# Kernel optimization log

Measured on AMD Instinct MI355X. Metric: run time of the kernel, lower is better.

## Reference

```python
import jax, jax.numpy as jnp
import numpy as np

B, S, DIM, H = 2, 2048, 1024, 16
DH = DIM // H


def setup_inputs() -> dict:
    key = jax.random.key(0)
    ks = jax.random.split(key, 12)
    sd = 0.02
    inp = {
        "query": jax.random.normal(ks[0], (B, S, DIM), jnp.float32),
        "key": jax.random.normal(ks[1], (B, S, DIM), jnp.float32),
        "value": jax.random.normal(ks[2], (B, S, DIM), jnp.float32),
        "pad_mask": jax.random.randint(ks[3], (B, 1, 1, S), 0, 2, jnp.int32),
        "training_status": 1,
        "Wq": jax.random.normal(ks[4], (DIM, DIM), jnp.float32) * sd,
        "bq": jnp.zeros((DIM,), jnp.float32),
        "Wk": jax.random.normal(ks[5], (DIM, DIM), jnp.float32) * sd,
        "bk": jnp.zeros((DIM,), jnp.float32),
        "Wv": jax.random.normal(ks[6], (DIM, DIM), jnp.float32) * sd,
        "bv": jnp.zeros((DIM,), jnp.float32),
        "Wf": jax.random.normal(ks[7], (DIM, DIM), jnp.float32) * sd,
        "bf": jnp.zeros((DIM,), jnp.float32),
    }
    return inp


def reference(query, key, value, pad_mask, training_status, Wq, bq, Wk, bk, Wv, bv, Wf, bf):
    b, s, _ = query.shape
    # projections, split heads -> [B, H, S, Dh]
    def split_heads(x):
        return x.reshape(b, -1, H, DH).transpose(0, 2, 1, 3)

    q = split_heads(query @ Wq + bq)
    k = split_heads(key @ Wk + bk)
    v = split_heads(value @ Wv + bv)

    # NOTE: original divides by sqrt(Dh) twice (explicit + self.scale) => /Dh
    scores = jnp.einsum("bhqd,bhkd->bhqk", q, k) / jnp.asarray(DH, q.dtype)
    if training_status:
        scores = jnp.where(pad_mask == 0, jnp.asarray(-1e9, scores.dtype), scores)
    attn = jax.nn.softmax(scores, axis=-1)
    out = jnp.einsum("bhqk,bhkd->bhqd", attn, v)  # [B,H,S,Dh]
    out = out.transpose(0, 2, 1, 3).reshape(b, s, DIM)
    return out @ Wf + bf
```

## Files before the change

kernel.cpp:

```cpp
#include <hip/hip_runtime.h>

#define Bn   2
#define Sn   2048
#define DIMn 1024
#define Hn   16
#define DHn  64

typedef unsigned short u16;
typedef unsigned int   u32;

typedef __attribute__((ext_vector_type(8))) __bf16 bf16x8;
typedef __attribute__((ext_vector_type(8))) float  f32x8v;
typedef __attribute__((ext_vector_type(4))) float  f32x4;

__device__ __forceinline__ u16 f2bf(float f) {
    union { float f; u32 u; } v; v.f = f;
    u32 r = v.u + 0x7fffu + ((v.u >> 16) & 1u);
    return (u16)(r >> 16);
}
__device__ __forceinline__ bf16x8 ldfrag(const u16* p) {
    union { uint4 u; bf16x8 v; } x;
    x.u = *(const uint4*)p;
    return x.v;
}
__device__ __forceinline__ uint4 pack8(const u16 h[8]) {
    uint4 r;
    r.x = (u32)h[0] | ((u32)h[1] << 16);
    r.y = (u32)h[2] | ((u32)h[3] << 16);
    r.z = (u32)h[4] | ((u32)h[5] << 16);
    r.w = (u32)h[6] | ((u32)h[7] << 16);
    return r;
}
__device__ __forceinline__ void gl_lds16(const void* g, void* l) {
    __builtin_amdgcn_global_load_lds(
        (const __attribute__((address_space(1))) void*)g,
        (__attribute__((address_space(3))) void*)l, 16, 0, 0);
}
__device__ __forceinline__ void barrier_nodrain() {
    asm volatile("" ::: "memory");
    __builtin_amdgcn_s_barrier();
    asm volatile("" ::: "memory");
}

__global__ __launch_bounds__(256) void prep_weights(
    const float* __restrict__ Wq, const float* __restrict__ Wk,
    const float* __restrict__ Wv, const float* __restrict__ Wf,
    u16* __restrict__ Wt)
{
    __shared__ __align__(16) float tile[64][68];
    const float* W = (blockIdx.z == 0) ? Wq : (blockIdx.z == 1) ? Wk
                   : (blockIdx.z == 2) ? Wv : Wf;
    const int t = threadIdx.x;
    const int n0 = blockIdx.x * 64, k0 = blockIdx.y * 64;
    const int rr = t >> 4, cc = (t & 15) * 4;
#pragma unroll
    for (int i = 0; i < 4; i++)
        *(float4*)&tile[rr + 16 * i][cc] =
            *(const float4*)(W + (size_t)(k0 + rr + 16 * i) * DIMn + n0 + cc);
    __syncthreads();
#pragma unroll
    for (int e = 0; e < 2; e++) {
        const int ci = 2 * t + e;
        const int nn = ci >> 3, kc = ci & 7;
        const int n = n0 + nn, k = k0 + kc * 8;
        u16 h[8];
#pragma unroll
        for (int j = 0; j < 8; j++) h[j] = f2bf(tile[kc * 8 + j][nn]);
        const int X = n >> 7, o = (n >> 4) & 7, l15 = n & 15;
        const int T = k >> 5, quad = (k >> 3) & 3;
        const size_t off =
            ((((size_t)(blockIdx.z * 8 + X) * 32 + T) * 8 + o) * 64 + quad * 16 + l15) * 8;
        *(uint4*)(Wt + off) = pack8(h);
    }
}

__global__ __launch_bounds__(256) void gemm_qkv(
    const float* __restrict__ Aq, const float* __restrict__ Ak,
    const float* __restrict__ Av, const u16* __restrict__ Wt,
    const float* __restrict__ bqp, const float* __restrict__ bkp,
    const float* __restrict__ bvp, u16* __restrict__ Qw,
    u16* __restrict__ Kw, u16* __restrict__ VwT)
{
    __shared__ union {
        struct { __align__(16) u16 Abf[2][4096];
                 __align__(16) u16 Bbf[2][4096]; } s;
        __align__(16) u16 Ep[32][144];
    } L;

    const int f = blockIdx.x;
    const int xcd = f & 7;
    const int q = f >> 3;
    const int z = q >> 5;
    const int rem = q & 31;
    const int yi = rem >> 3, x = rem & 7;
    const int y = xcd * 4 + yi;
    const int m0 = y * 128, n0 = x * 128;

    const float* A    = (z == 0) ? Aq  : (z == 1) ? Ak  : Av;
    const float* bias = (z == 0) ? bqp : (z == 1) ? bkp : bvp;

    const int t = threadIdx.x;
    const int lane = t & 63, wave = t >> 6;
    const int quad = lane >> 4, l15 = lane & 15;
    const int wm = wave >> 1, wn = wave & 1;

    const float* baseA[2];
#pragma unroll
    for (int s = 0; s < 2; s++)
        baseA[s] = A + (size_t)(m0 + (wave * 2 + s) * 16 + l15) * DIMn + quad * 8;
    const u16* baseB[2];
#pragma unroll
    for (int s = 0; s < 2; s++)
        baseB[s] = Wt + ((size_t)((z * 8 + x) * 32) * 8 + (wave * 2 + s)) * 512 + lane * 8;

    auto LOADA = [&](int tt, uint4 (&ar)[4]) {
#pragma unroll
        for (int s = 0; s < 2; s++) {
            const float* p = baseA[s] + tt * 32;
            ar[2 * s]     = *(const uint4*)(p);
            ar[2 * s + 1] = *(const uint4*)(p + 4);
        }
    };
    auto STAGEB = [&](int tt, int buf) {
#pragma unroll
        for (int s = 0; s < 2; s++)
            gl_lds16(baseB[s] + (size_t)tt * 4096, &L.s.Bbf[buf][(wave * 2 + s) * 512]);
    };
    auto CVTWRITE = [&](uint4 (&ar)[4], int buf) {
#pragma unroll
        for (int s = 0; s < 2; s++) {
            union { uint4 u[2]; f32x8v f; } cv;
            cv.u[0] = ar[2 * s]; cv.u[1] = ar[2 * s + 1];
            union { bf16x8 v; uint4 u; } hv;
            hv.v = __builtin_convertvector(cv.f, bf16x8);
            *(uint4*)&L.s.Abf[buf][(wave * 2 + s) * 512 + lane * 8] = hv.u;
        }
    };

    f32x4 acc[4][4];
#pragma unroll
    for (int i = 0; i < 4; i++)
#pragma unroll
        for (int j = 0; j < 4; j++) acc[i][j] = (f32x4){0.f, 0.f, 0.f, 0.f};

    const int NT = DIMn / 32;
    uint4 ra[4], rb[4];
    LOADA(0, ra); STAGEB(0, 0);
    LOADA(1, rb); STAGEB(1, 1);

    auto ITER = [&](int tt, uint4 (&ar)[4], int buf) {
        if (tt < NT - 1) asm volatile("s_waitcnt vmcnt(6)" ::: "memory");
        else             asm volatile("s_waitcnt vmcnt(0)" ::: "memory");
        CVTWRITE(ar, buf);
        asm volatile("s_waitcnt lgkmcnt(0)" ::: "memory");
        barrier_nodrain();

        bf16x8 a[4], b[4];
#pragma unroll
        for (int i = 0; i < 4; i++)
            a[i] = ldfrag(&L.s.Abf[buf][((wm * 4 + i) * 4 + quad) * 128 + l15 * 8]);
#pragma unroll
        for (int j = 0; j < 4; j++)
            b[j] = ldfrag(&L.s.Bbf[buf][((wn * 4 + j) * 4 + quad) * 128 + l15 * 8]);
#pragma unroll
        for (int i = 0; i < 4; i++)
#pragma unroll
            for (int j = 0; j < 4; j++)
                acc[i][j] = __builtin_amdgcn_mfma_f32_16x16x32_bf16(a[i], b[j], acc[i][j], 0, 0, 0);

        asm volatile("s_waitcnt lgkmcnt(0)" ::: "memory");
        barrier_nodrain();
        if (tt + 2 < NT) { LOADA(tt + 2, ar); STAGEB(tt + 2, buf); }
    };
    for (int tt = 0; tt < NT; tt += 2) { ITER(tt, ra, 0); ITER(tt + 1, rb, 1); }

    float bv[4];
#pragma unroll
    for (int j = 0; j < 4; j++) bv[j] = bias[n0 + wn * 64 + j * 16 + l15];

    const int bb = y >> 4;

    if (z == 0) {
#pragma unroll
        for (int i = 0; i < 4; i++) {
            __syncthreads();
#pragma unroll
            for (int j = 0; j < 4; j++)
#pragma unroll
                for (int r = 0; r < 4; r++)
                    L.Ep[wm * 16 + quad * 4 + r][wn * 64 + j * 16 + l15] =
                        f2bf(acc[i][j][r] + bv[j]);
            __syncthreads();
#pragma unroll
            for (int e = 0; e < 2; e++) {
                const int ci = t + 256 * e;
                const int row = ci >> 4, c = ci & 15;
                const uint4 v = *(const uint4*)&L.Ep[row][c * 8];
                const int m = m0 + (row >> 4) * 64 + i * 16 + (row & 15);
                const int ss = m & 2047;
                const int n = n0 + c * 8;
                const int hh = n >> 6, dd = n & 63;
                *(uint4*)(Qw + ((size_t)(bb * Hn + hh) * Sn + ss) * DHn + dd) = v;
            }
        }
    } else if (z == 1) {
#pragma unroll
        for (int i = 0; i < 4; i++) {
            __syncthreads();
#pragma unroll
            for (int j = 0; j < 4; j++)
#pragma unroll
                for (int r = 0; r < 4; r++)
                    L.Ep[wm * 16 + quad * 4 + r][wn * 64 + j * 16 + l15] =
                        f2bf(acc[i][j][r] + bv[j]);
            __syncthreads();
#pragma unroll
            for (int e2 = 0; e2 < 2; e2++) {
                const int tid = t + 256 * e2;
                const int l15o = tid & 15;
                const int qo   = (tid >> 4) & 3;
                const int k1   = (tid >> 6) & 1;
                const int c3   = (tid >> 7) & 1;
                const int w    = (tid >> 8) & 1;
                const int c    = c3 * 8 + k1 * 4 + qo;
                const uint4 v = *(const uint4*)&L.Ep[w * 16 + l15o][c * 8];
                const int ss = (m0 & 2047) + w * 64 + i * 16 + l15o;
                const int hh = (n0 + c * 8) >> 6;
                const int jt = ss >> 6;
                const int o  = i * 2 + k1;
                const size_t off =
                    ((((size_t)(bb * Hn + hh) * 32 + jt) * 8 + o) * 64 + qo * 16 + l15o) * 8;
                *(uint4*)(Kw + off) = v;
            }
        }
    } else {
#pragma unroll
        for (int j = 0; j < 4; j++) {
            __syncthreads();
#pragma unroll
            for (int i = 0; i < 4; i++) {
                u16 h4[4];
#pragma unroll
                for (int r = 0; r < 4; r++) h4[r] = f2bf(acc[i][j][r] + bv[j]);
                uint2 pk;
                pk.x = (u32)h4[0] | ((u32)h4[1] << 16);
                pk.y = (u32)h4[2] | ((u32)h4[3] << 16);
                *(uint2*)&L.Ep[wn * 16 + l15][wm * 64 + i * 16 + quad * 4] = pk;
            }
            __syncthreads();
#pragma unroll
            for (int e2 = 0; e2 < 2; e2++) {
                const int tid = t + 256 * e2;
                const int l15o = tid & 15;
                const int qo   = (tid >> 4) & 3;
                const int k1   = (tid >> 6) & 1;
                const int c3   = (tid >> 7) & 1;
                const int w    = (tid >> 8) & 1;
                const int c    = c3 * 8 + k1 * 4 + qo;
                const uint4 v = *(const uint4*)&L.Ep[w * 16 + l15o][c * 8];
                const int n  = n0 + w * 64 + j * 16 + l15o;
                const int hh = n >> 6;
                const int jt = ((m0 & 2047) >> 6) + c3;
                const int o  = j * 2 + k1;
                const size_t off =
                    ((((size_t)(bb * Hn + hh) * 32 + jt) * 8 + o) * 64 + qo * 16 + l15o) * 8;
                *(uint4*)(VwT + off) = v;
            }
        }
    }
}

__global__ __launch_bounds__(256) void gemm_final(
    const u16* __restrict__ A, const u16* __restrict__ Bt,
    const float* __restrict__ bias, float* __restrict__ out)
{
    __shared__ __align__(16) u16 Abf[2][16 * 512];
    __shared__ __align__(16) u16 Bbf[2][8 * 512];

    const int f = blockIdx.x;
    const int xcd = f & 7, q = f >> 3;
    const int y = xcd * 4 + (q >> 4);
    const int x = q & 15;
    const int m0 = y * 128, n0 = x * 64;
    const int bb = y >> 4;
    const int jtb = (y & 15) * 2;

    const int t = threadIdx.x;
    const int lane = t & 63, wave = t >> 6;
    const int quad = lane >> 4, l15 = lane & 15;
    const int wm = wave >> 1, wn = wave & 1;

    const u16* baseA[4];
#pragma unroll
    for (int s = 0; s < 4; s++) {
        const int c = wave * 4 + s;
        const int g = c >> 1, dsub = c & 1;
        const int jt2 = g >> 2, sub16 = g & 3;
        baseA[s] = A + (((size_t)(bb * Hn) * 32 + jtb + jt2) * 8 + (sub16 * 2 + dsub)) * 512
                     + lane * 8;
    }
    const u16* baseB[2];
#pragma unroll
    for (int s = 0; s < 2; s++) {
        const int cb = wave * 2 + s;
        const int os = cb >> 1, ksub = cb & 1;
        baseB[s] = Bt + (((size_t)(x >> 1) * 32 + ksub) * 8 + ((x & 1) * 4 + os)) * 512
                      + lane * 8;
    }

    auto STAGE = [&](int tt, int buf) {
#pragma unroll
        for (int s = 0; s < 4; s++)
            gl_lds16(baseA[s] + (size_t)tt * 131072, &Abf[buf][(wave * 4 + s) * 512]);
#pragma unroll
        for (int s = 0; s < 2; s++)
            gl_lds16(baseB[s] + (size_t)tt * 8192, &Bbf[buf][(wave * 2 + s) * 512]);
    };

    f32x4 acc[4][2];
#pragma unroll
    for (int i = 0; i < 4; i++)
#pragma unroll
        for (int j = 0; j < 2; j++) acc[i][j] = (f32x4){0.f, 0.f, 0.f, 0.f};

    const int NT = 16;
    STAGE(0, 0);
    STAGE(1, 1);

    for (int tt = 0; tt < NT; ++tt) {
        const int buf = tt & 1;
        if (tt < NT - 1) asm volatile("s_waitcnt vmcnt(6)" ::: "memory");
        else             asm volatile("s_waitcnt vmcnt(0)" ::: "memory");
        barrier_nodrain();

        bf16x8 a[4][2], b[2][2];
#pragma unroll
        for (int i = 0; i < 4; i++)
#pragma unroll
            for (int ks = 0; ks < 2; ks++) {
                const int c = (wm * 4 + i) * 2 + ks;
                a[i][ks] = ldfrag(&Abf[buf][c * 512 + (quad * 16 + l15) * 8]);
            }
#pragma unroll
        for (int j = 0; j < 2; j++)
#pragma unroll
            for (int ks = 0; ks < 2; ks++) {
                const int cb = (wn * 2 + j) * 2 + ks;
                b[j][ks] = ldfrag(&Bbf[buf][cb * 512 + (quad * 16 + l15) * 8]);
            }
#pragma unroll
        for (int i = 0; i < 4; i++)
#pragma unroll
            for (int j = 0; j < 2; j++)
#pragma unroll
                for (int ks = 0; ks < 2; ks++)
                    acc[i][j] = __builtin_amdgcn_mfma_f32_16x16x32_bf16(
                        a[i][ks], b[j][ks], acc[i][j], 0, 0, 0);

        asm volatile("s_waitcnt lgkmcnt(0)" ::: "memory");
        barrier_nodrain();
        if (tt + 2 < NT) STAGE(tt + 2, buf);
    }

    float bv[2];
#pragma unroll
    for (int j = 0; j < 2; j++) bv[j] = bias[n0 + wn * 32 + j * 16 + l15];

#pragma unroll
    for (int i = 0; i < 4; i++)
#pragma unroll
        for (int j = 0; j < 2; j++) {
            const int n = n0 + wn * 32 + j * 16 + l15;
#pragma unroll
            for (int r = 0; r < 4; r++) {
                const int m = m0 + wm * 64 + i * 16 + quad * 4 + r;
                out[(size_t)m * DIMn + n] = acc[i][j][r] + bv[j];
            }
        }
}

__global__ __launch_bounds__(256) void attn_mfma(
    const u16* __restrict__ Qw, const u16* __restrict__ Kw,
    const u16* __restrict__ VwT, const int* __restrict__ mask,
    const int* __restrict__ tstat, u16* __restrict__ Aw)
{
    __shared__ __align__(16) u16 Kbf[2][32 * 128];
    __shared__ __align__(16) u16 Vbf[2][32 * 128];
    __shared__ __align__(16) u16 Ps[64 * 64];

    const int f = blockIdx.x;
    const int xcd = f & 7, q = f >> 3;
    const int p = xcd * 4 + (q >> 5);
    const int qt = q & 31;
    const int b = p >> 4, h = p & 15;
    const int q0 = qt * 64;

    const int t = threadIdx.x;
    const int lane = t & 63, wave = t >> 6;
    const int quad = lane >> 4, l15 = lane & 15;
    const bool use_mask = (tstat[0] != 0);
    const size_t slab = (size_t)(b * Hn + h) * Sn * DHn;

    const size_t hbase = (size_t)(b * Hn + h) * 32 * 8 * 512;
    const u16* baseK[2];
    const u16* baseV[2];
#pragma unroll
    for (int s = 0; s < 2; s++) {
        const int o = wave * 2 + s;
        baseK[s] = Kw  + hbase + (size_t)o * 512 + lane * 8;
        baseV[s] = VwT + hbase + (size_t)o * 512 + lane * 8;
    }

    {
        const int4* msrc4 = (const int4*)(mask + (size_t)b * Sn);
        int4* mdst4 = (int4*)&Kbf[0][0];
        mdst4[t]       = msrc4[t];
        mdst4[t + 256] = msrc4[t + 256];
    }
    bf16x8 aq[2];
#pragma unroll
    for (int ks = 0; ks < 2; ks++) {
        union { uint4 u; bf16x8 v; } xx;
        xx.u = *(const uint4*)(Qw + slab + (size_t)(q0 + wave * 16 + l15) * DHn + ks * 32 + quad * 8);
        aq[ks] = xx.v;
    }
    __syncthreads();

    u32 mw0 = 0, mw1 = 0, mw2 = 0, mw3 = 0;
    {
        const int* ml = (const int*)&Kbf[0][0];
#pragma unroll
        for (int k = 0; k < 128; k++) {
            const u32 bit = (ml[k * 16 + l15] != 0) ? 1u : 0u;
            if (k < 32)      mw0 |= bit << k;
            else if (k < 64) mw1 |= bit << (k - 32);
            else if (k < 96) mw2 |= bit << (k - 64);
            else             mw3 |= bit << (k - 96);
        }
    }
    __syncthreads();

    auto STAGE = [&](int tt, int buf) {
#pragma unroll
        for (int s = 0; s < 2; s++) {
            gl_lds16(baseK[s] + (size_t)tt * 4096, &Kbf[buf][(wave * 8 + s * 4) * 128]);
            gl_lds16(baseV[s] + (size_t)tt * 4096, &Vbf[buf][(wave * 8 + s * 4) * 128]);
        }
    };

    float lsum[4] = {0.f, 0.f, 0.f, 0.f};
    f32x4 O[4];
#pragma unroll
    for (int dt = 0; dt < 4; dt++) O[dt] = (f32x4){0.f, 0.f, 0.f, 0.f};

    const int NT = Sn / 64;
    STAGE(0, 0);
    STAGE(1, 1);

#pragma unroll 8
    for (int tt = 0; tt < NT; ++tt) {
        const int buf = tt & 1;
        if (tt < NT - 1) asm volatile("s_waitcnt vmcnt(4)" ::: "memory");
        else             asm volatile("s_waitcnt vmcnt(0)" ::: "memory");
        barrier_nodrain();

        f32x4 s[4];
#pragma unroll
        for (int ct = 0; ct < 4; ct++) s[ct] = (f32x4){0.f, 0.f, 0.f, 0.f};
#pragma unroll
        for (int ct = 0; ct < 4; ct++)
#pragma unroll
            for (int ks = 0; ks < 2; ks++) {
                const bf16x8 bk = ldfrag(&Kbf[buf][(ct * 8 + ks * 4 + quad) * 128 + l15 * 8]);
                s[ct] = __builtin_amdgcn_mfma_f32_16x16x32_bf16(aq[ks], bk, s[ct], 0, 0, 0);
            }

        const int wsel = tt >> 3;
        const u32 cw = (wsel == 0) ? mw0 : (wsel == 1) ? mw1 : (wsel == 2) ? mw2 : mw3;
        const int sh = (tt & 7) * 4;
        float badd[4];
#pragma unroll
        for (int ct = 0; ct < 4; ct++)
            badd[ct] = (!use_mask || ((cw >> (sh + ct)) & 1u)) ? 0.0f : -1e9f;

#pragma unroll
        for (int ct = 0; ct < 4; ct++)
#pragma unroll
            for (int r = 0; r < 4; r++) {
                const float pp = __expf(fmaf(s[ct][r], 1.0f / 64.0f, badd[ct]));
                lsum[r] += pp;
                const int prow = wave * 16 + quad * 4 + r;
                Ps[prow * 64 + ((ct * 16 + l15) ^ ((prow & 7) << 3))] = f2bf(pp);
            }
        asm volatile("s_waitcnt lgkmcnt(0)" ::: "memory");

        bf16x8 pa[2];
        const int rrow = wave * 16 + l15;
#pragma unroll
        for (int kc = 0; kc < 2; kc++)
            pa[kc] = ldfrag(&Ps[rrow * 64 + ((kc * 32 + quad * 8) ^ ((l15 & 7) << 3))]);
#pragma unroll
        for (int dt = 0; dt < 4; dt++)
#pragma unroll
            for (int kc = 0; kc < 2; kc++) {
                const bf16x8 bvv = ldfrag(&Vbf[buf][(dt * 8 + kc * 4 + quad) * 128 + l15 * 8]);
                O[dt] = __builtin_amdgcn_mfma_f32_16x16x32_bf16(pa[kc], bvv, O[dt], 0, 0, 0);
            }

        asm volatile("s_waitcnt lgkmcnt(0)" ::: "memory");
        barrier_nodrain();
        if (tt + 2 < NT) STAGE(tt + 2, buf);
    }

#pragma unroll
    for (int r = 0; r < 4; r++) {
#pragma unroll
        for (int off = 1; off < 16; off <<= 1) lsum[r] += __shfl_xor(lsum[r], off);
    }
    float linv[4];
#pragma unroll
    for (int r = 0; r < 4; r++) linv[r] = 1.0f / fmaxf(lsum[r], 1e-30f);

    __syncthreads();
#pragma unroll
    for (int r = 0; r < 4; r++)
#pragma unroll
        for (int dt = 0; dt < 4; dt++)
            Ps[(wave * 16 + quad * 4 + r) * 64 + dt * 16 + l15] = f2bf(O[dt][r] * linv[r]);
    __syncthreads();
    const size_t cbase = ((size_t)(b * Hn + h) * 32 + qt) * 4096;
#pragma unroll
    for (int e2 = 0; e2 < 2; e2++) {
        const int tid = t + 256 * e2;
        const int row = tid >> 3, cg = tid & 7;
        const int sub16 = row >> 4, dsub = cg >> 2, quadk = cg & 3;
        const uint4 v = *(const uint4*)&Ps[row * 64 + cg * 8];
        *(uint4*)(Aw + cbase + (size_t)(sub16 * 2 + dsub) * 512
                  + (quadk * 16 + (row & 15)) * 8) = v;
    }
}

extern "C" void kernel_launch(void* const* d_in, const int* in_sizes, int n_in,
                              void* d_out, int out_size, void* d_ws, size_t ws_size,
                              hipStream_t stream) {
    const float* query = (const float*)d_in[0];
    const float* key   = (const float*)d_in[1];
    const float* value = (const float*)d_in[2];
    const int*   pmask = (const int*)d_in[3];
    const int*   tstat = (const int*)d_in[4];
    const float* Wq  = (const float*)d_in[5];
    const float* bq  = (const float*)d_in[6];
    const float* Wk  = (const float*)d_in[7];
    const float* bk  = (const float*)d_in[8];
    const float* Wv  = (const float*)d_in[9];
    const float* bv  = (const float*)d_in[10];
    const float* Wf  = (const float*)d_in[11];
    const float* bfb = (const float*)d_in[12];
    float* outp = (float*)d_out;

    const size_t NT = (size_t)Bn * Sn * DIMn;
    u16* Qw  = (u16*)d_ws;
    u16* Kw  = Qw + NT;
    u16* VwT = Kw + NT;
    u16* Wt  = VwT + NT;
    const size_t WSZ = (size_t)DIMn * DIMn;

    prep_weights<<<dim3(16, 16, 4), 256, 0, stream>>>(Wq, Wk, Wv, Wf, Wt);

    gemm_qkv<<<768, 256, 0, stream>>>(query, key, value, Wt, bq, bk, bv, Qw, Kw, VwT);

    attn_mfma<<<1024, 256, 0, stream>>>(Qw, Kw, VwT, pmask, tstat, Qw);

    gemm_final<<<512, 256, 0, stream>>>(Qw, Wt + 3 * WSZ, bfb, outp);
}
```

Before: 268.3 us.

## Coalesce QKV A loads, triple-buffer final GEMM, split softmax/PV in attention

The QKV projection now loads fp32 A rows with a coalesced lane mapping: eight lanes cover 32 contiguous floats. It converts four floats at a time and scatters them into the fragment layout in LDS. The final GEMM moves from double to triple buffering, with deeper vmcnt waits to hide more global-to-LDS latency. The attention kernel switches to exp2 with the log2e constant folded in, lowers unroll from 8 to 2, and splits the P-write/PV MFMA into two halves so MFMA overlaps exp work; the extra LDS and scattered 8-byte LDS writes may cost occupancy or bank conflicts.

```diff
diff --git a/kernel.cpp b/kernel.cpp
--- a/kernel.cpp
+++ b/kernel.cpp
@@ -10,6 +10,7 @@
 typedef unsigned int   u32;
 
 typedef __attribute__((ext_vector_type(8))) __bf16 bf16x8;
+typedef __attribute__((ext_vector_type(4))) __bf16 bf16x4;
 typedef __attribute__((ext_vector_type(8))) float  f32x8v;
 typedef __attribute__((ext_vector_type(4))) float  f32x4;
 
@@ -103,11 +104,12 @@
     const int lane = t & 63, wave = t >> 6;
     const int quad = lane >> 4, l15 = lane & 15;
     const int wm = wave >> 1, wn = wave & 1;
+    const int r8 = lane >> 3, c8 = lane & 7;
 
     const float* baseA[2];
 #pragma unroll
     for (int s = 0; s < 2; s++)
-        baseA[s] = A + (size_t)(m0 + (wave * 2 + s) * 16 + l15) * DIMn + quad * 8;
+        baseA[s] = A + (size_t)(m0 + (wave * 2 + s) * 16 + r8) * DIMn + c8 * 4;
     const u16* baseB[2];
 #pragma unroll
     for (int s = 0; s < 2; s++)
@@ -115,11 +117,10 @@
 
     auto LOADA = [&](int tt, uint4 (&ar)[4]) {
 #pragma unroll
-        for (int s = 0; s < 2; s++) {
-            const float* p = baseA[s] + tt * 32;
-            ar[2 * s]     = *(const uint4*)(p);
-            ar[2 * s + 1] = *(const uint4*)(p + 4);
-        }
+        for (int s = 0; s < 2; s++)
+#pragma unroll
+            for (int h = 0; h < 2; h++)
+                ar[2 * s + h] = *(const uint4*)(baseA[s] + (size_t)h * 8 * DIMn + tt * 32);
     };
     auto STAGEB = [&](int tt, int buf) {
 #pragma unroll
@@ -128,13 +129,15 @@
     };
     auto CVTWRITE = [&](uint4 (&ar)[4], int buf) {
 #pragma unroll
-        for (int s = 0; s < 2; s++) {
-            union { uint4 u[2]; f32x8v f; } cv;
-            cv.u[0] = ar[2 * s]; cv.u[1] = ar[2 * s + 1];
-            union { bf16x8 v; uint4 u; } hv;
-            hv.v = __builtin_convertvector(cv.f, bf16x8);
-            *(uint4*)&L.s.Abf[buf][(wave * 2 + s) * 512 + lane * 8] = hv.u;
-        }
+        for (int s = 0; s < 2; s++)
+#pragma unroll
+            for (int h = 0; h < 2; h++) {
+                union { uint4 u; f32x4 f; } cv; cv.u = ar[2 * s + h];
+                union { bf16x4 v; uint2 u; } hv;
+                hv.v = __builtin_convertvector(cv.f, bf16x4);
+                *(uint2*)&L.s.Abf[buf][(wave * 2 + s) * 512 +
+                    ((c8 >> 1) * 16 + r8 + h * 8) * 8 + (c8 & 1) * 4] = hv.u;
+            }
     };
 
     f32x4 acc[4][4];
@@ -182,7 +185,7 @@
 
     if (z == 0) {
 #pragma unroll
-        for (int i = 0; i < 4; i++) {
+    for (int i = 0; i < 4; i++) {
             __syncthreads();
 #pragma unroll
             for (int j = 0; j < 4; j++)
@@ -274,8 +277,8 @@
     const u16* __restrict__ A, const u16* __restrict__ Bt,
     const float* __restrict__ bias, float* __restrict__ out)
 {
-    __shared__ __align__(16) u16 Abf[2][16 * 512];
-    __shared__ __align__(16) u16 Bbf[2][8 * 512];
+    __shared__ __align__(16) u16 Abf[3][16 * 512];
+    __shared__ __align__(16) u16 Bbf[3][8 * 512];
 
     const int f = blockIdx.x;
     const int xcd = f & 7, q = f >> 3;
@@ -326,11 +329,13 @@
     const int NT = 16;
     STAGE(0, 0);
     STAGE(1, 1);
-
+    STAGE(2, 2);
+
+    int buf = 0;
     for (int tt = 0; tt < NT; ++tt) {
-        const int buf = tt & 1;
-        if (tt < NT - 1) asm volatile("s_waitcnt vmcnt(6)" ::: "memory");
-        else             asm volatile("s_waitcnt vmcnt(0)" ::: "memory");
+        if (tt < NT - 2)       asm volatile("s_waitcnt vmcnt(12)" ::: "memory");
+        else if (tt == NT - 2) asm volatile("s_waitcnt vmcnt(6)" ::: "memory");
+        else                   asm volatile("s_waitcnt vmcnt(0)" ::: "memory");
         barrier_nodrain();
 
         bf16x8 a[4][2], b[2][2];
@@ -359,7 +364,8 @@
 
         asm volatile("s_waitcnt lgkmcnt(0)" ::: "memory");
         barrier_nodrain();
-        if (tt + 2 < NT) STAGE(tt + 2, buf);
+        if (tt + 3 < NT) STAGE(tt + 3, buf);
+        buf = (buf == 2) ? 0 : buf + 1;
     }
 
     float bv[2];
@@ -453,11 +459,12 @@
 #pragma unroll
     for (int dt = 0; dt < 4; dt++) O[dt] = (f32x4){0.f, 0.f, 0.f, 0.f};
 
+    const float C1 = 1.44269504f / 64.0f;
     const int NT = Sn / 64;
     STAGE(0, 0);
     STAGE(1, 1);
 
-#pragma unroll 8
+#pragma unroll 2
     for (int tt = 0; tt < NT; ++tt) {
         const int buf = tt & 1;
         if (tt < NT - 1) asm volatile("s_waitcnt vmcnt(4)" ::: "memory");
@@ -481,31 +488,44 @@
         float badd[4];
 #pragma unroll
         for (int ct = 0; ct < 4; ct++)
-            badd[ct] = (!use_mask || ((cw >> (sh + ct)) & 1u)) ? 0.0f : -1e9f;
-
-#pragma unroll
-        for (int ct = 0; ct < 4; ct++)
+            badd[ct] = (!use_mask || ((cw >> (sh + ct)) & 1u)) ? 0.0f : -1.44269504e9f;
+
+        const int prowb = wave * 16 + quad * 4;
+        const int rrow = wave * 16 + l15;
+
+#pragma unroll
+        for (int ct = 0; ct < 2; ct++)
 #pragma unroll
             for (int r = 0; r < 4; r++) {
-                const float pp = __expf(fmaf(s[ct][r], 1.0f / 64.0f, badd[ct]));
+                const float pp = __builtin_amdgcn_exp2f(fmaf(s[ct][r], C1, badd[ct]));
                 lsum[r] += pp;
-                const int prow = wave * 16 + quad * 4 + r;
-                Ps[prow * 64 + ((ct * 16 + l15) ^ ((prow & 7) << 3))] = f2bf(pp);
+                Ps[(prowb + r) * 64 + ((ct * 16 + l15) ^ (((prowb + r) & 7) << 3))] = f2bf(pp);
             }
         asm volatile("s_waitcnt lgkmcnt(0)" ::: "memory");
-
-        bf16x8 pa[2];
-        const int rrow = wave * 16 + l15;
-#pragma unroll
-        for (int kc = 0; kc < 2; kc++)
-            pa[kc] = ldfrag(&Ps[rrow * 64 + ((kc * 32 + quad * 8) ^ ((l15 & 7) << 3))]);
-#pragma unroll
-        for (int dt = 0; dt < 4; dt++)
-#pragma unroll
-            for (int kc = 0; kc < 2; kc++) {
-                const bf16x8 bvv = ldfrag(&Vbf[buf][(dt * 8 + kc * 4 + quad) * 128 + l15 * 8]);
-                O[dt] = __builtin_amdgcn_mfma_f32_16x16x32_bf16(pa[kc], bvv, O[dt], 0, 0, 0);
-            }
+        const bf16x8 pa0 = ldfrag(&Ps[rrow * 64 + ((quad * 8) ^ ((l15 & 7) << 3))]);
+
+#pragma unroll
+        for (int ct = 2; ct < 4; ct++)
+#pragma unroll
+            for (int r = 0; r < 4; r++) {
+                const float pp = __builtin_amdgcn_exp2f(fmaf(s[ct][r], C1, badd[ct]));
+                lsum[r] += pp;
+                Ps[(prowb + r) * 64 + ((ct * 16 + l15) ^ (((prowb + r) & 7) << 3))] = f2bf(pp);
+            }
+
+#pragma unroll
+        for (int dt = 0; dt < 4; dt++) {
+            const bf16x8 bvv = ldfrag(&Vbf[buf][(dt * 8 + quad) * 128 + l15 * 8]);
+            O[dt] = __builtin_amdgcn_mfma_f32_16x16x32_bf16(pa0, bvv, O[dt], 0, 0, 0);
+        }
+        asm volatile("s_waitcnt lgkmcnt(0)" ::: "memory");
+        const bf16x8 pa1 = ldfrag(&Ps[rrow * 64 + ((32 + quad * 8) ^ ((l15 & 7) << 3))]);
+
+#pragma unroll
+        for (int dt = 0; dt < 4; dt++) {
+            const bf16x8 bvv = ldfrag(&Vbf[buf][(dt * 8 + 4 + quad) * 128 + l15 * 8]);
+            O[dt] = __builtin_amdgcn_mfma_f32_16x16x32_bf16(pa1, bvv, O[dt], 0, 0, 0);
+        }
 
         asm volatile("s_waitcnt lgkmcnt(0)" ::: "memory");
         barrier_nodrain();
```

After: 246.9 us. 1.09x faster.
